# Optimization experiments

Measured on AMD Instinct MI355X. Metric: run time of the kernel, lower is better.

Reference implementation:

```python
import jax, jax.numpy as jnp
import numpy as np

NEG_SLOPE = 0.2
EPS = 1e-16
HEADS1, OUT1 = 4, 32
HEADS2, OUT2 = 1, 32


def _gat_conv(x, W, a_src, a_dst, bias, src, dst, num_nodes, heads, out_c, concat):
    # x: [N, F_in], W: [F_in, heads*out_c], a_*: [heads, out_c]
    h = (x @ W).reshape(num_nodes, heads, out_c)            # [N, H, C]
    alpha_src = (h * a_src).sum(-1)                          # [N, H]
    alpha_dst = (h * a_dst).sum(-1)                          # [N, H]
    e = jax.nn.leaky_relu(alpha_src[src] + alpha_dst[dst], NEG_SLOPE)  # [E, H]
    # softmax over incoming edges of each destination node (PyG softmax)
    m = jax.ops.segment_max(e, dst, num_segments=num_nodes)
    ex = jnp.exp(e - m[dst])
    s = jax.ops.segment_sum(ex, dst, num_segments=num_nodes)
    alpha = ex / (s[dst] + EPS)                              # [E, H]
    out = jax.ops.segment_sum(h[src] * alpha[:, :, None], dst,
                              num_segments=num_nodes)        # [N, H, C]
    out = out.reshape(num_nodes, heads * out_c) if concat else out.mean(axis=1)
    return out + bias


def setup_inputs() -> dict:
    key = jax.random.key(0)
    ks = jax.random.split(key, 10)
    N, E, F_IN = 50000, 1600000, 128
    sc = 0.1
    return {
        "x": jax.random.normal(ks[0], (N, F_IN), jnp.float32),
        "edge_index": jax.random.randint(ks[1], (2, E), 0, N, jnp.int32),
        "W1": jax.random.normal(ks[2], (F_IN, HEADS1 * OUT1), jnp.float32) * sc,
        "a_src1": jax.random.normal(ks[3], (HEADS1, OUT1), jnp.float32) * sc,
        "a_dst1": jax.random.normal(ks[4], (HEADS1, OUT1), jnp.float32) * sc,
        "b1": jax.random.normal(ks[5], (HEADS1 * OUT1,), jnp.float32) * sc,
        "W2": jax.random.normal(ks[6], (HEADS1 * OUT1, HEADS2 * OUT2), jnp.float32) * sc,
        "a_src2": jax.random.normal(ks[7], (HEADS2, OUT2), jnp.float32) * sc,
        "a_dst2": jax.random.normal(ks[8], (HEADS2, OUT2), jnp.float32) * sc,
        "b2": jax.random.normal(ks[9], (OUT2,), jnp.float32) * sc,
    }


def reference(x, edge_index, W1, a_src1, a_dst1, b1, W2, a_src2, a_dst2, b2):
    N = x.shape[0]
    # PyG GATConv default add_self_loops=True
    loops = jnp.arange(N, dtype=edge_index.dtype)
    src = jnp.concatenate([edge_index[0], loops])
    dst = jnp.concatenate([edge_index[1], loops])
    h = _gat_conv(x, W1, a_src1, a_dst1, b1, src, dst, N, HEADS1, OUT1, True)
    h = jax.nn.elu(h)
    return _gat_conv(h, W2, a_src2, a_dst2, b2, src, dst, N, HEADS2, OUT2, False)
```

## Files before the change

kernel.cpp:

```cpp
#include <hip/hip_runtime.h>
#include <math.h>

#define NEG_SLOPE 0.2f
#define EPSV 1e-16f
#define NPART 8

typedef _Float16 half4 __attribute__((ext_vector_type(4)));
typedef _Float16 half8 __attribute__((ext_vector_type(8)));
typedef float floatx2 __attribute__((ext_vector_type(2)));
typedef float f32x4 __attribute__((ext_vector_type(4)));


__global__ void k_scan_blk(const int* __restrict__ degp, int N,
                           int* __restrict__ rowptr, int* __restrict__ bsum){
    int b = blockIdx.x, t = threadIdx.x;
    int base = b * 1024 + t * 4;
    int v[4];
    #pragma unroll
    for (int j = 0; j < 4; j++){
        int n = base + j, s = 0;
        if (n < N){
            #pragma unroll
            for (int p = 0; p < NPART; p++) s += degp[p * N + n];
        }
        v[j] = s;
    }
    int s = v[0] + v[1] + v[2] + v[3];
    int lane = t & 63, wid = t >> 6;
    int x = s;
    #pragma unroll
    for (int off = 1; off < 64; off <<= 1){
        int y = __shfl_up(x, off, 64);
        if (lane >= off) x += y;
    }
    __shared__ int ws[4];
    if (lane == 63) ws[wid] = x;
    __syncthreads();
    int woff = 0;
    for (int w = 0; w < wid; w++) woff += ws[w];
    int run = woff + x - s;
    #pragma unroll
    for (int j = 0; j < 4; j++){
        if (base + j < N) rowptr[base + j] = run;
        run += v[j];
    }
    if (t == 255) bsum[b] = woff + x;
}

__global__ void k_finalize(const int* __restrict__ bsum, const int* __restrict__ degp,
                           int N, int ET,
                           int* __restrict__ rowptr, int* __restrict__ poff){
    int b = blockIdx.x, t = threadIdx.x;
    int n = b * 256 + t;
    int chunk = (b * 256) >> 10;
    int off = 0;
    for (int c = 0; c < chunk; c++) off += bsum[c];
    if (n < N){
        int r = rowptr[n] + off;
        rowptr[n] = r;
        int run = r;
        #pragma unroll
        for (int p = 0; p < NPART; p++){
            poff[p * N + n] = run;
            run += degp[p * N + n];
        }
    }
    if (n == 0) rowptr[N] = ET;
}

__launch_bounds__(256)
__global__ void k_scatter2(const int* __restrict__ ei, int E, int ET, int N,
                           const int* __restrict__ poff,
                           const unsigned short* __restrict__ rank,
                           int* __restrict__ csr_src){
    int i = blockIdx.x * 256 + threadIdx.x;
    if (i >= ET) return;
    int s, d;
    if (i < E){ s = ei[i]; d = ei[E + i]; } else { s = i - E; d = s; }
    int pr = rank[i];
    int p = pr >> 13, r = pr & 0x1FFF;
    csr_src[poff[p * N + d] + r] = s;
}


__global__ void k_pack(const float* __restrict__ W1, const float* __restrict__ a_src1,
                       const float* __restrict__ a_dst1,
                       const float* __restrict__ W2, const float* __restrict__ a_src2,
                       const float* __restrict__ a_dst2,
                       _Float16* __restrict__ W1f, _Float16* __restrict__ Uf,
                       _Float16* __restrict__ W2f, _Float16* __restrict__ U2f){
    int b = blockIdx.x, t = threadIdx.x;
    if (b < 32){
        #pragma unroll
        for (int i = 0; i < 2; i++){
            int idx = t + 256 * i;
            int jj = idx & 7, ln = idx >> 3;
            int kt = b & 3, ct = b >> 2;
            int k = kt * 32 + (ln >> 4) * 8 + jj;
            int col = ct * 16 + (ln & 15);
            W1f[b * 512 + idx] = (_Float16)W1[k * 128 + col];
        }
        return;
    }
    if (b == 32){
        __shared__ float U[128 * 8];
        if (t < 128){
            #pragma unroll
            for (int h = 0; h < 4; h++){
                float s = 0.f, d = 0.f;
                for (int cc = 0; cc < 32; cc++){
                    float w = W1[t * 128 + h * 32 + cc];
                    s += w * a_src1[h * 32 + cc];
                    d += w * a_dst1[h * 32 + cc];
                }
                U[t * 8 + h]     = s;
                U[t * 8 + h + 4] = d;
            }
        }
        __syncthreads();
        for (int idx = t; idx < 4 * 64 * 8; idx += 256){
            int jj = idx & 7, ln = (idx >> 3) & 63, kt = idx >> 9;
            int k = kt * 32 + (ln >> 4) * 8 + jj;
            int col = ln & 15;
            Uf[idx] = (_Float16)(col < 8 ? U[k * 8 + col] : 0.f);
        }
        return;
    }
    if (b < 41){
        int tb = b - 33;
        #pragma unroll
        for (int i = 0; i < 2; i++){
            int idx = t + 256 * i;
            int jj = idx & 7, ln = idx >> 3;
            int kt = tb & 3, ct = tb >> 2;
            int k = kt * 32 + (ln >> 4) * 8 + jj;
            int col = ct * 16 + (ln & 15);
            W2f[tb * 512 + idx] = (_Float16)W2[k * 32 + col];
        }
        return;
    }
    __shared__ float U2[128 * 2];
    if (t < 128){
        float s = 0.f, d = 0.f;
        for (int cc = 0; cc < 32; cc++){
            float w = W2[t * 32 + cc];
            s += w * a_src2[cc];
            d += w * a_dst2[cc];
        }
        U2[t * 2]     = s;
        U2[t * 2 + 1] = d;
    }
    __syncthreads();
    for (int idx = t; idx < 4 * 64 * 8; idx += 256){
        int jj = idx & 7, ln = (idx >> 3) & 63, kt = idx >> 9;
        int k = kt * 32 + (ln >> 4) * 8 + jj;
        int col = ln & 15;
        U2f[idx] = (_Float16)(col < 2 ? U2[k * 2 + col] : 0.f);
    }
}


__launch_bounds__(256)
__global__ void k_gemm1_hist(const float* __restrict__ x, const _Float16* __restrict__ W1f,
                             const _Float16* __restrict__ Uf,
                             _Float16* __restrict__ h1h, float* __restrict__ asrc1,
                             float* __restrict__ adst1, int N, int GH,
                             const int* __restrict__ ei, int E, int ET,
                             unsigned int* __restrict__ degp, unsigned short* __restrict__ rank){
    int t = threadIdx.x;
    if ((int)blockIdx.x < GH){
        int p = __builtin_amdgcn_s_getreg((3 << 11) | 20) & 7;
        int base = blockIdx.x * 4096 + t;
        int d[16];
        #pragma unroll
        for (int j = 0; j < 16; j++){
            int i = base + j * 256;
            d[j] = (i < ET) ? ((i < E) ? ei[E + i] : (i - E)) : 0;
        }
        unsigned r[16];
        #pragma unroll
        for (int j = 0; j < 16; j++){
            int i = base + j * 256;
            r[j] = 0;
            if (i < ET)
                r[j] = __hip_atomic_fetch_add(&degp[(size_t)p * N + d[j]], 1u,
                           __ATOMIC_RELAXED, __HIP_MEMORY_SCOPE_WORKGROUP);
        }
        #pragma unroll
        for (int j = 0; j < 16; j++){
            int i = base + j * 256;
            if (i < ET) rank[i] = (unsigned short)((p << 13) | r[j]);
        }
        return;
    }
    int gb = blockIdx.x - GH;
    int w = t >> 6, lane = t & 63;
    int arow = gb * 64 + w * 16 + (lane & 15);
    bool arow_ok = (arow < N);
    const float4* xr = (const float4*)&x[(size_t)(arow_ok ? arow : 0) << 7];
    const half8* Wf = (const half8*)W1f;
    const half8* Uv = (const half8*)Uf;

    f32x4 acc[8];
    #pragma unroll
    for (int c = 0; c < 8; c++) acc[c] = (f32x4)0.f;
    f32x4 accA = (f32x4)0.f;

    #pragma unroll
    for (int kt = 0; kt < 4; kt++){
        half8 af;
        if (arow_ok){
            float4 p0 = xr[kt * 8 + (lane >> 4) * 2];
            float4 p1 = xr[kt * 8 + (lane >> 4) * 2 + 1];
            af[0] = (_Float16)p0.x; af[1] = (_Float16)p0.y;
            af[2] = (_Float16)p0.z; af[3] = (_Float16)p0.w;
            af[4] = (_Float16)p1.x; af[5] = (_Float16)p1.y;
            af[6] = (_Float16)p1.z; af[7] = (_Float16)p1.w;
        } else {
            af[0] = (_Float16)0.f; af[1] = (_Float16)0.f;
            af[2] = (_Float16)0.f; af[3] = (_Float16)0.f;
            af[4] = (_Float16)0.f; af[5] = (_Float16)0.f;
            af[6] = (_Float16)0.f; af[7] = (_Float16)0.f;
        }
        #pragma unroll
        for (int ct = 0; ct < 8; ct++){
            half8 bf = Wf[(ct * 4 + kt) * 64 + lane];
            acc[ct] = __builtin_amdgcn_mfma_f32_16x16x32_f16(af, bf, acc[ct], 0, 0, 0);
        }
        half8 uf = Uv[kt * 64 + lane];
        accA = __builtin_amdgcn_mfma_f32_16x16x32_f16(af, uf, accA, 0, 0, 0);
    }

    int g = lane >> 4, j = lane & 15;
    int rowbase = gb * 64 + w * 16 + g * 4;
    #pragma unroll
    for (int r = 0; r < 4; r++){
        int n = rowbase + r;
        if (n >= N) continue;
        _Float16* hrow = &h1h[(size_t)n << 7];
        #pragma unroll
        for (int ct = 0; ct < 8; ct++)
            hrow[ct * 16 + j] = (_Float16)acc[ct][r];
        float av = accA[r];
        if (j < 4)            asrc1[n * 4 + j]       = av;
        else if (j < 8)       adst1[n * 4 + (j - 4)] = av;
    }
}


__launch_bounds__(256)
__global__ void k_agg1(const int* __restrict__ rowptr, const int* __restrict__ csr_src,
                       const float* __restrict__ asrc1, const float* __restrict__ adst1,
                       const _Float16* __restrict__ h1h,
                       const float* __restrict__ b1, float* __restrict__ x2, int N){
    int t = threadIdx.x;
    int lane = t & 63;
    int g = lane >> 4, l = lane & 15, head = l >> 2;
    int n = blockIdx.x * 16 + ((t >> 6) << 2) + g;
    bool valid = (n < N);
    int nn = valid ? n : 0;
    int start = rowptr[nn], end = rowptr[nn + 1];
    float adn = adst1[(nn << 2) + head];
    const char* hb = (const char*)h1h;
    const char* ab = (const char*)asrc1;
    int hoff = l << 4;
    int aoff = head << 2;
    floatx2 r0[4], r1[4], r2[4], r3[4];
    #pragma unroll
    for (int j = 0; j < 4; j++){
        r0[j] = (floatx2)0.f; r1[j] = (floatx2)0.f;
        r2[j] = (floatx2)0.f; r3[j] = (floatx2)0.f;
    }
    float s0a = 0.f, s1a = 0.f, s2a = 0.f, s3a = 0.f;
    int i = start;
    for (; i + 3 < end; i += 4){
        int sa = csr_src[i];
        int sb = csr_src[i + 1];
        int sc = csr_src[i + 2];
        int sd = csr_src[i + 3];
        float ea = *(const float*)(ab + (sa << 4) + aoff) + adn;
        float eb = *(const float*)(ab + (sb << 4) + aoff) + adn;
        float ec = *(const float*)(ab + (sc << 4) + aoff) + adn;
        float ed = *(const float*)(ab + (sd << 4) + aoff) + adn;
        ea = fmaxf(ea, NEG_SLOPE * ea);
        eb = fmaxf(eb, NEG_SLOPE * eb);
        ec = fmaxf(ec, NEG_SLOPE * ec);
        ed = fmaxf(ed, NEG_SLOPE * ed);
        float wa = __expf(ea);
        float wb = __expf(eb);
        float wc = __expf(ec);
        float wd = __expf(ed);
        half8 ha = *(const half8*)(hb + (sa << 8) + hoff);
        half8 hbv = *(const half8*)(hb + (sb << 8) + hoff);
        half8 hcv = *(const half8*)(hb + (sc << 8) + hoff);
        half8 hdv = *(const half8*)(hb + (sd << 8) + hoff);
        s0a += wa; s1a += wb; s2a += wc; s3a += wd;
        floatx2 wa2 = {wa, wa}, wb2 = {wb, wb}, wc2 = {wc, wc}, wd2 = {wd, wd};
        #pragma unroll
        for (int j = 0; j < 4; j++){
            floatx2 ca = {(float)ha[2*j], (float)ha[2*j+1]};
            floatx2 cb = {(float)hbv[2*j], (float)hbv[2*j+1]};
            floatx2 cc = {(float)hcv[2*j], (float)hcv[2*j+1]};
            floatx2 cd = {(float)hdv[2*j], (float)hdv[2*j+1]};
            r0[j] = wa2 * ca + r0[j];
            r1[j] = wb2 * cb + r1[j];
            r2[j] = wc2 * cc + r2[j];
            r3[j] = wd2 * cd + r3[j];
        }
    }
    for (; i < end; i++){
        int sa = csr_src[i];
        float ea = *(const float*)(ab + (sa << 4) + aoff) + adn;
        ea = fmaxf(ea, NEG_SLOPE * ea);
        float wa = __expf(ea);
        half8 ha = *(const half8*)(hb + (sa << 8) + hoff);
        s0a += wa;
        floatx2 wa2 = {wa, wa};
        #pragma unroll
        for (int j = 0; j < 4; j++){
            floatx2 ca = {(float)ha[2*j], (float)ha[2*j+1]};
            r0[j] = wa2 * ca + r0[j];
        }
    }
    if (valid){
        float ssum = (s0a + s1a) + (s2a + s3a);
        float inv = 1.f / (ssum + EPSV);
        float o[8];
        #pragma unroll
        for (int j = 0; j < 4; j++){
            floatx2 c = (r0[j] + r1[j]) + (r2[j] + r3[j]);
            float v0 = c.x * inv + b1[l * 8 + 2*j];
            float v1 = c.y * inv + b1[l * 8 + 2*j + 1];
            o[2*j]   = (v0 > 0.f) ? v0 : expm1f(v0);
            o[2*j+1] = (v1 > 0.f) ? v1 : expm1f(v1);
        }
        float4 o0 = {o[0], o[1], o[2], o[3]};
        float4 o1 = {o[4], o[5], o[6], o[7]};
        *(float4*)&x2[((size_t)n << 7) + (l << 3)]     = o0;
        *(float4*)&x2[((size_t)n << 7) + (l << 3) + 4] = o1;
    }
}


__launch_bounds__(256)
__global__ void k_gemm2(const float* __restrict__ x2, const _Float16* __restrict__ W2f,
                        const _Float16* __restrict__ U2f,
                        _Float16* __restrict__ h2h, float* __restrict__ asrc2,
                        float* __restrict__ adst2, int N){
    int t = threadIdx.x;
    int w = t >> 6, lane = t & 63;
    int arow = blockIdx.x * 64 + w * 16 + (lane & 15);
    bool arow_ok = (arow < N);
    const float4* xr = (const float4*)&x2[(size_t)(arow_ok ? arow : 0) << 7];
    const half8* Wf = (const half8*)W2f;
    const half8* Uv = (const half8*)U2f;

    f32x4 acc0 = (f32x4)0.f, acc1 = (f32x4)0.f, accA = (f32x4)0.f;

    #pragma unroll
    for (int kt = 0; kt < 4; kt++){
        half8 af;
        if (arow_ok){
            float4 p0 = xr[kt * 8 + (lane >> 4) * 2];
            float4 p1 = xr[kt * 8 + (lane >> 4) * 2 + 1];
            af[0] = (_Float16)p0.x; af[1] = (_Float16)p0.y;
            af[2] = (_Float16)p0.z; af[3] = (_Float16)p0.w;
            af[4] = (_Float16)p1.x; af[5] = (_Float16)p1.y;
            af[6] = (_Float16)p1.z; af[7] = (_Float16)p1.w;
        } else {
            af[0] = (_Float16)0.f; af[1] = (_Float16)0.f;
            af[2] = (_Float16)0.f; af[3] = (_Float16)0.f;
            af[4] = (_Float16)0.f; af[5] = (_Float16)0.f;
            af[6] = (_Float16)0.f; af[7] = (_Float16)0.f;
        }
        half8 b0 = Wf[(0 * 4 + kt) * 64 + lane];
        half8 b1v = Wf[(1 * 4 + kt) * 64 + lane];
        half8 uf = Uv[kt * 64 + lane];
        acc0 = __builtin_amdgcn_mfma_f32_16x16x32_f16(af, b0, acc0, 0, 0, 0);
        acc1 = __builtin_amdgcn_mfma_f32_16x16x32_f16(af, b1v, acc1, 0, 0, 0);
        accA = __builtin_amdgcn_mfma_f32_16x16x32_f16(af, uf, accA, 0, 0, 0);
    }

    int g = lane >> 4, j = lane & 15;
    int rowbase = blockIdx.x * 64 + w * 16 + g * 4;
    #pragma unroll
    for (int r = 0; r < 4; r++){
        int n = rowbase + r;
        if (n >= N) continue;
        _Float16* hrow = &h2h[(size_t)n << 5];
        hrow[j]      = (_Float16)acc0[r];
        hrow[16 + j] = (_Float16)acc1[r];
        float av = accA[r];
        if (j == 0)      asrc2[n] = av;
        else if (j == 1) adst2[n] = av;
    }
}


__launch_bounds__(256)
__global__ void k_agg2(const int* __restrict__ rowptr, const int* __restrict__ csr_src,
                       const float* __restrict__ asrc2, const float* __restrict__ adst2,
                       const _Float16* __restrict__ h2h,
                       const float* __restrict__ b2, float* __restrict__ out, int N){
    int t = threadIdx.x;
    int lane = t & 63;
    int g = lane >> 3, l = lane & 7;
    int n = blockIdx.x * 32 + ((t >> 6) << 3) + g;
    bool valid = (n < N);
    int nn = valid ? n : 0;
    int start = rowptr[nn], end = rowptr[nn + 1];
    float adn = adst2[nn];
    const char* hb = (const char*)h2h;
    const char* ab = (const char*)asrc2;
    int hoff = l << 3;
    floatx2 a0[2], a1[2], a2[2], a3[2];
    a0[0] = (floatx2)0.f; a0[1] = (floatx2)0.f;
    a1[0] = (floatx2)0.f; a1[1] = (floatx2)0.f;
    a2[0] = (floatx2)0.f; a2[1] = (floatx2)0.f;
    a3[0] = (floatx2)0.f; a3[1] = (floatx2)0.f;
    float s0a = 0.f, s1a = 0.f, s2a = 0.f, s3a = 0.f;
    int i = start;
    for (; i + 3 < end; i += 4){
        int sa = csr_src[i];
        int sb = csr_src[i + 1];
        int sc = csr_src[i + 2];
        int sd = csr_src[i + 3];
        float ea = *(const float*)(ab + (sa << 2)) + adn;
        float eb = *(const float*)(ab + (sb << 2)) + adn;
        float ec = *(const float*)(ab + (sc << 2)) + adn;
        float ed = *(const float*)(ab + (sd << 2)) + adn;
        ea = fmaxf(ea, NEG_SLOPE * ea);
        eb = fmaxf(eb, NEG_SLOPE * eb);
        ec = fmaxf(ec, NEG_SLOPE * ec);
        ed = fmaxf(ed, NEG_SLOPE * ed);
        float wa = __expf(ea);
        float wb = __expf(eb);
        float wc = __expf(ec);
        float wd = __expf(ed);
        half4 ha = *(const half4*)(hb + (sa << 6) + hoff);
        half4 hbv = *(const half4*)(hb + (sb << 6) + hoff);
        half4 hcv = *(const half4*)(hb + (sc << 6) + hoff);
        half4 hdv = *(const half4*)(hb + (sd << 6) + hoff);
        s0a += wa; s1a += wb; s2a += wc; s3a += wd;
        floatx2 wa2 = {wa, wa}, wb2 = {wb, wb}, wc2 = {wc, wc}, wd2 = {wd, wd};
        floatx2 ca0 = {(float)ha.x, (float)ha.y},  ca1 = {(float)ha.z, (float)ha.w};
        floatx2 cb0 = {(float)hbv.x, (float)hbv.y}, cb1 = {(float)hbv.z, (float)hbv.w};
        floatx2 cc0 = {(float)hcv.x, (float)hcv.y}, cc1 = {(float)hcv.z, (float)hcv.w};
        floatx2 cd0 = {(float)hdv.x, (float)hdv.y}, cd1 = {(float)hdv.z, (float)hdv.w};
        a0[0] = wa2 * ca0 + a0[0]; a0[1] = wa2 * ca1 + a0[1];
        a1[0] = wb2 * cb0 + a1[0]; a1[1] = wb2 * cb1 + a1[1];
        a2[0] = wc2 * cc0 + a2[0]; a2[1] = wc2 * cc1 + a2[1];
        a3[0] = wd2 * cd0 + a3[0]; a3[1] = wd2 * cd1 + a3[1];
    }
    for (; i < end; i++){
        int sa = csr_src[i];
        float ea = *(const float*)(ab + (sa << 2)) + adn;
        ea = fmaxf(ea, NEG_SLOPE * ea);
        float wa = __expf(ea);
        half4 ha = *(const half4*)(hb + (sa << 6) + hoff);
        s0a += wa;
        floatx2 wa2 = {wa, wa};
        floatx2 ca0 = {(float)ha.x, (float)ha.y}, ca1 = {(float)ha.z, (float)ha.w};
        a0[0] = wa2 * ca0 + a0[0]; a0[1] = wa2 * ca1 + a0[1];
    }
    if (valid){
        floatx2 m0 = (a0[0] + a1[0]) + (a2[0] + a3[0]);
        floatx2 m1 = (a0[1] + a1[1]) + (a2[1] + a3[1]);
        float ssum = (s0a + s1a) + (s2a + s3a);
        float inv = 1.f / (ssum + EPSV);
        const float4 b4 = *(const float4*)&b2[l * 4];
        float4 o;
        o.x = m0.x * inv + b4.x; o.y = m0.y * inv + b4.y;
        o.z = m1.x * inv + b4.z; o.w = m1.y * inv + b4.w;
        *(float4*)&out[((size_t)n << 5) + (l << 2)] = o;
    }
}


extern "C" void kernel_launch(void* const* d_in, const int* in_sizes, int n_in,
                              void* d_out, int out_size, void* d_ws, size_t ws_size,
                              hipStream_t stream){
    const float* x      = (const float*)d_in[0];
    const int*   ei     = (const int*)  d_in[1];
    const float* W1     = (const float*)d_in[2];
    const float* a_src1 = (const float*)d_in[3];
    const float* a_dst1 = (const float*)d_in[4];
    const float* b1     = (const float*)d_in[5];
    const float* W2     = (const float*)d_in[6];
    const float* a_src2 = (const float*)d_in[7];
    const float* a_dst2 = (const float*)d_in[8];
    const float* b2     = (const float*)d_in[9];
    float* out = (float*)d_out;

    int N  = in_sizes[0] / 128;
    int E  = in_sizes[1] / 2;
    int ET = E + N;
    int nScanBlk = (N + 1023) / 1024;
    int G  = (ET + 255) / 256;
    int GH = (ET + 4095) / 4096;
    int nGemmBlk = (N + 63) / 64;

    char* ws = (char*)d_ws;
    size_t off = 0;
    auto alloc = [&](size_t bytes) -> char* {
        char* p = ws + off;
        off += (bytes + 255) & ~(size_t)255;
        return p;
    };
    int*            degp    = (int*)           alloc((size_t)NPART * N * 4);
    int*            rowptr  = (int*)           alloc((size_t)(N + 1) * 4);
    int*            bsum    = (int*)           alloc((size_t)nScanBlk * 4);
    unsigned short* rank    = (unsigned short*)alloc((size_t)ET * 2);
    int*            poff    = (int*)           alloc((size_t)NPART * N * 4);
    int*            csr_src = (int*)           alloc((size_t)ET * 4);
    _Float16*       h1h     = (_Float16*)      alloc((size_t)N * 128 * 2);
    float*          x2      = (float*)         alloc((size_t)N * 128 * 4);
    float*          asrc1   = (float*)         alloc((size_t)N * 4 * 4);
    float*          adst1   = (float*)         alloc((size_t)N * 4 * 4);
    _Float16*       h2h     = (_Float16*)      alloc((size_t)N * 32 * 2);
    float*          asrc2   = (float*)         alloc((size_t)N * 4);
    float*          adst2   = (float*)         alloc((size_t)N * 4);
    _Float16*       W1f     = (_Float16*)      alloc((size_t)32 * 512 * 2);
    _Float16*       Uf      = (_Float16*)      alloc((size_t)4 * 512 * 2);
    _Float16*       W2f     = (_Float16*)      alloc((size_t)8 * 512 * 2);
    _Float16*       U2f     = (_Float16*)      alloc((size_t)4 * 512 * 2);

    hipMemsetAsync(degp, 0, (size_t)NPART * N * 4, stream);
    hipLaunchKernelGGL(k_pack,       dim3(42), dim3(256), 0, stream,
                       W1, a_src1, a_dst1, W2, a_src2, a_dst2, W1f, Uf, W2f, U2f);
    hipLaunchKernelGGL(k_gemm1_hist, dim3(GH + nGemmBlk), dim3(256), 0, stream,
                       x, W1f, Uf, h1h, asrc1, adst1, N, GH,
                       ei, E, ET, (unsigned int*)degp, rank);
    hipLaunchKernelGGL(k_scan_blk,  dim3(nScanBlk), dim3(256), 0, stream, degp, N, rowptr, bsum);
    hipLaunchKernelGGL(k_finalize,  dim3((N + 255) / 256), dim3(256), 0, stream, bsum, degp, N, ET, rowptr, poff);
    hipLaunchKernelGGL(k_scatter2,  dim3(G), dim3(256), 0, stream, ei, E, ET, N, poff, rank, csr_src);
    hipLaunchKernelGGL(k_agg1,      dim3((N + 15) / 16), dim3(256), 0, stream, rowptr, csr_src, asrc1, adst1, h1h, b1, x2, N);
    hipLaunchKernelGGL(k_gemm2,     dim3((N + 63) / 64), dim3(256), 0, stream, x2, W2f, U2f, h2h, asrc2, adst2, N);
    hipLaunchKernelGGL(k_agg2,      dim3((N + 31) / 32), dim3(256), 0, stream, rowptr, csr_src, asrc2, adst2, h2h, b2, out, N);
}
```

Measured before the change: 295.5 us.

## Fuse layer-1 aggregation with layer-2 GEMM via shared-memory tile

The layer-1 aggregation kernel now writes its ELU output rows into an LDS tile instead of global memory. After a barrier, three waves run the layer-2 MFMA projection and attention-vector products on that tile, which removes the x2 buffer and the separate gemm2 launch. The gemm1/histogram kernel also swaps block ordering so GEMM blocks get the lower block indices. In exchange, a quarter of the waves sit idle during the fused GEMM phase, and the extra LDS per block may reduce occupancy of the gather loop.

After: 296.0 us. Within noise of the previous version (+0.2%).

```diff
diff --git a/kernel.cpp b/kernel.cpp
--- a/kernel.cpp
+++ b/kernel.cpp
@@ -164,13 +164,13 @@
 __global__ void k_gemm1_hist(const float* __restrict__ x, const _Float16* __restrict__ W1f,
                              const _Float16* __restrict__ Uf,
                              _Float16* __restrict__ h1h, float* __restrict__ asrc1,
-                             float* __restrict__ adst1, int N, int GH,
+                             float* __restrict__ adst1, int N, int nGemmBlk,
                              const int* __restrict__ ei, int E, int ET,
                              unsigned int* __restrict__ degp, unsigned short* __restrict__ rank){
     int t = threadIdx.x;
-    if ((int)blockIdx.x < GH){
+    if ((int)blockIdx.x >= nGemmBlk){
         int p = __builtin_amdgcn_s_getreg((3 << 11) | 20) & 7;
-        int base = blockIdx.x * 4096 + t;
+        int base = (blockIdx.x - nGemmBlk) * 4096 + t;
         int d[16];
         #pragma unroll
         for (int j = 0; j < 16; j++){
@@ -193,7 +193,7 @@
         }
         return;
     }
-    int gb = blockIdx.x - GH;
+    int gb = blockIdx.x;
     int w = t >> 6, lane = t & 63;
     int arow = gb * 64 + w * 16 + (lane & 15);
     bool arow_ok = (arow < N);
@@ -249,14 +249,18 @@
 
 
 __launch_bounds__(256)
-__global__ void k_agg1(const int* __restrict__ rowptr, const int* __restrict__ csr_src,
-                       const float* __restrict__ asrc1, const float* __restrict__ adst1,
-                       const _Float16* __restrict__ h1h,
-                       const float* __restrict__ b1, float* __restrict__ x2, int N){
+__global__ void k_agg1g2(const int* __restrict__ rowptr, const int* __restrict__ csr_src,
+                         const float* __restrict__ asrc1, const float* __restrict__ adst1,
+                         const _Float16* __restrict__ h1h, const float* __restrict__ b1,
+                         const _Float16* __restrict__ W2f, const _Float16* __restrict__ U2f,
+                         _Float16* __restrict__ h2h, float* __restrict__ asrc2,
+                         float* __restrict__ adst2, int N){
+    __shared__ float xl[16 * 132];
     int t = threadIdx.x;
     int lane = t & 63;
     int g = lane >> 4, l = lane & 15, head = l >> 2;
-    int n = blockIdx.x * 16 + ((t >> 6) << 2) + g;
+    int nloc = ((t >> 6) << 2) + g;
+    int n = blockIdx.x * 16 + nloc;
     bool valid = (n < N);
     int nn = valid ? n : 0;
     int start = rowptr[nn], end = rowptr[nn + 1];
@@ -322,77 +326,46 @@
             r0[j] = wa2 * ca + r0[j];
         }
     }
-    if (valid){
+    {
         float ssum = (s0a + s1a) + (s2a + s3a);
         float inv = 1.f / (ssum + EPSV);
-        float o[8];
+        float* xrow = &xl[nloc * 132 + (l << 3)];
         #pragma unroll
         for (int j = 0; j < 4; j++){
             floatx2 c = (r0[j] + r1[j]) + (r2[j] + r3[j]);
             float v0 = c.x * inv + b1[l * 8 + 2*j];
             float v1 = c.y * inv + b1[l * 8 + 2*j + 1];
-            o[2*j]   = (v0 > 0.f) ? v0 : expm1f(v0);
-            o[2*j+1] = (v1 > 0.f) ? v1 : expm1f(v1);
-        }
-        float4 o0 = {o[0], o[1], o[2], o[3]};
-        float4 o1 = {o[4], o[5], o[6], o[7]};
-        *(float4*)&x2[((size_t)n << 7) + (l << 3)]     = o0;
-        *(float4*)&x2[((size_t)n << 7) + (l << 3) + 4] = o1;
-    }
-}
-
-
-__launch_bounds__(256)
-__global__ void k_gemm2(const float* __restrict__ x2, const _Float16* __restrict__ W2f,
-                        const _Float16* __restrict__ U2f,
-                        _Float16* __restrict__ h2h, float* __restrict__ asrc2,
-                        float* __restrict__ adst2, int N){
-    int t = threadIdx.x;
-    int w = t >> 6, lane = t & 63;
-    int arow = blockIdx.x * 64 + w * 16 + (lane & 15);
-    bool arow_ok = (arow < N);
-    const float4* xr = (const float4*)&x2[(size_t)(arow_ok ? arow : 0) << 7];
-    const half8* Wf = (const half8*)W2f;
-    const half8* Uv = (const half8*)U2f;
-
-    f32x4 acc0 = (f32x4)0.f, acc1 = (f32x4)0.f, accA = (f32x4)0.f;
-
+            xrow[2*j]   = (v0 > 0.f) ? v0 : expm1f(v0);
+            xrow[2*j+1] = (v1 > 0.f) ? v1 : expm1f(v1);
+        }
+    }
+    __syncthreads();
+    int w = t >> 6;
+    if (w >= 3) return;
+    const half8* Bf = (w < 2) ? (const half8*)W2f + (size_t)w * 4 * 64
+                              : (const half8*)U2f;
+    f32x4 acc = (f32x4)0.f;
     #pragma unroll
     for (int kt = 0; kt < 4; kt++){
+        const float* xr = &xl[(lane & 15) * 132 + kt * 32 + (lane >> 4) * 8];
         half8 af;
-        if (arow_ok){
-            float4 p0 = xr[kt * 8 + (lane >> 4) * 2];
-            float4 p1 = xr[kt * 8 + (lane >> 4) * 2 + 1];
-            af[0] = (_Float16)p0.x; af[1] = (_Float16)p0.y;
-            af[2] = (_Float16)p0.z; af[3] = (_Float16)p0.w;
-            af[4] = (_Float16)p1.x; af[5] = (_Float16)p1.y;
-            af[6] = (_Float16)p1.z; af[7] = (_Float16)p1.w;
+        #pragma unroll
+        for (int jj = 0; jj < 8; jj++) af[jj] = (_Float16)xr[jj];
+        half8 bf = Bf[kt * 64 + lane];
+        acc = __builtin_amdgcn_mfma_f32_16x16x32_f16(af, bf, acc, 0, 0, 0);
+    }
+    int g2 = lane >> 4, j2 = lane & 15;
+    #pragma unroll
+    for (int r = 0; r < 4; r++){
+        int nl = g2 * 4 + r;
+        int no = blockIdx.x * 16 + nl;
+        if (no >= N) continue;
+        if (w < 2){
+            h2h[((size_t)no << 5) + w * 16 + j2] = (_Float16)acc[r];
         } else {
-            af[0] = (_Float16)0.f; af[1] = (_Float16)0.f;
-            af[2] = (_Float16)0.f; af[3] = (_Float16)0.f;
-            af[4] = (_Float16)0.f; af[5] = (_Float16)0.f;
-            af[6] = (_Float16)0.f; af[7] = (_Float16)0.f;
-        }
-        half8 b0 = Wf[(0 * 4 + kt) * 64 + lane];
-        half8 b1v = Wf[(1 * 4 + kt) * 64 + lane];
-        half8 uf = Uv[kt * 64 + lane];
-        acc0 = __builtin_amdgcn_mfma_f32_16x16x32_f16(af, b0, acc0, 0, 0, 0);
-        acc1 = __builtin_amdgcn_mfma_f32_16x16x32_f16(af, b1v, acc1, 0, 0, 0);
-        accA = __builtin_amdgcn_mfma_f32_16x16x32_f16(af, uf, accA, 0, 0, 0);
-    }
-
-    int g = lane >> 4, j = lane & 15;
-    int rowbase = blockIdx.x * 64 + w * 16 + g * 4;
-    #pragma unroll
-    for (int r = 0; r < 4; r++){
-        int n = rowbase + r;
-        if (n >= N) continue;
-        _Float16* hrow = &h2h[(size_t)n << 5];
-        hrow[j]      = (_Float16)acc0[r];
-        hrow[16 + j] = (_Float16)acc1[r];
-        float av = accA[r];
-        if (j == 0)      asrc2[n] = av;
-        else if (j == 1) adst2[n] = av;
+            if (j2 == 0)      asrc2[no] = acc[r];
+            else if (j2 == 1) adst2[no] = acc[r];
+        }
     }
 }
 
@@ -514,7 +487,6 @@
     int*            poff    = (int*)           alloc((size_t)NPART * N * 4);
     int*            csr_src = (int*)           alloc((size_t)ET * 4);
     _Float16*       h1h     = (_Float16*)      alloc((size_t)N * 128 * 2);
-    float*          x2      = (float*)         alloc((size_t)N * 128 * 4);
     float*          asrc1   = (float*)         alloc((size_t)N * 4 * 4);
     float*          adst1   = (float*)         alloc((size_t)N * 4 * 4);
     _Float16*       h2h     = (_Float16*)      alloc((size_t)N * 32 * 2);
@@ -528,13 +500,14 @@
     hipMemsetAsync(degp, 0, (size_t)NPART * N * 4, stream);
     hipLaunchKernelGGL(k_pack,       dim3(42), dim3(256), 0, stream,
                        W1, a_src1, a_dst1, W2, a_src2, a_dst2, W1f, Uf, W2f, U2f);
-    hipLaunchKernelGGL(k_gemm1_hist, dim3(GH + nGemmBlk), dim3(256), 0, stream,
-                       x, W1f, Uf, h1h, asrc1, adst1, N, GH,
+    hipLaunchKernelGGL(k_gemm1_hist, dim3(nGemmBlk + GH), dim3(256), 0, stream,
+                       x, W1f, Uf, h1h, asrc1, adst1, N, nGemmBlk,
                        ei, E, ET, (unsigned int*)degp, rank);
     hipLaunchKernelGGL(k_scan_blk,  dim3(nScanBlk), dim3(256), 0, stream, degp, N, rowptr, bsum);
     hipLaunchKernelGGL(k_finalize,  dim3((N + 255) / 256), dim3(256), 0, stream, bsum, degp, N, ET, rowptr, poff);
     hipLaunchKernelGGL(k_scatter2,  dim3(G), dim3(256), 0, stream, ei, E, ET, N, poff, rank, csr_src);
-    hipLaunchKernelGGL(k_agg1,      dim3((N + 15) / 16), dim3(256), 0, stream, rowptr, csr_src, asrc1, adst1, h1h, b1, x2, N);
-    hipLaunchKernelGGL(k_gemm2,     dim3((N + 63) / 64), dim3(256), 0, stream, x2, W2f, U2f, h2h, asrc2, adst2, N);
+    hipLaunchKernelGGL(k_agg1g2,    dim3((N + 15) / 16), dim3(256), 0, stream,
+                       rowptr, csr_src, asrc1, adst1, h1h, b1, W2f, U2f,
+                       h2h, asrc2, adst2, N);
     hipLaunchKernelGGL(k_agg2,      dim3((N + 31) / 32), dim3(256), 0, stream, rowptr, csr_src, asrc2, adst2, h2h, b2, out, N);
 }
```
